# Optimization experiments

Hardware: AMD Instinct MI355X
Metric: run time of the kernel (lower is better)

The kernel has to match this reference:

```python
import jax, jax.numpy as jnp
import numpy as np

N = 100000
E = 1600000
H = 128
C = 40
BN_EPS = 1e-5


def setup_inputs() -> dict:
    key = jax.random.key(0)
    ks = jax.random.split(key, 8)
    x = jax.random.normal(ks[0], (N, H), dtype=jnp.float32)
    edge_index = jax.random.randint(ks[1], (2, E), 0, N, dtype=jnp.int64)
    # 3 GCN blocks (input + 2 hidden), all [H -> H] since in_channels == hidden_channels
    bn_gamma = jnp.ones((3, H), dtype=jnp.float32)
    bn_beta = jnp.zeros((3, H), dtype=jnp.float32)
    W = jax.random.normal(ks[2], (3, H, H), dtype=jnp.float32) / np.sqrt(H)
    b = jnp.zeros((3, H), dtype=jnp.float32)
    Wo = jax.random.normal(ks[3], (H, C), dtype=jnp.float32) / np.sqrt(H)
    bo = jnp.zeros((C,), dtype=jnp.float32)
    return {"x": x, "edge_index": edge_index, "bn_gamma": bn_gamma,
            "bn_beta": bn_beta, "W": W, "b": b, "Wo": Wo, "bo": bo}


def _gcn_norm(edge_index):
    # add self-loops, compute symmetric normalization deg^-1/2 * deg^-1/2
    loop = jnp.arange(N, dtype=edge_index.dtype)
    src = jnp.concatenate([edge_index[0], loop])  # [E+N]
    dst = jnp.concatenate([edge_index[1], loop])
    deg = jax.ops.segment_sum(jnp.ones_like(dst, dtype=jnp.float32), dst, num_segments=N)
    dinv = jnp.where(deg > 0, jax.lax.rsqrt(deg), 0.0)
    norm = dinv[src] * dinv[dst]  # [E+N]
    return src, dst, norm


def _block(x, src, dst, norm, gamma, beta, Wl, bl):
    # Dropout(p=0.6) in eval mode -> identity
    # BatchNorm (batch statistics, biased var, eps=1e-5)
    mean = jnp.mean(x, axis=0)
    var = jnp.mean(jnp.square(x - mean), axis=0)
    x = gamma * (x - mean) * jax.lax.rsqrt(var + BN_EPS) + beta
    # GCNConv: linear transform then normalized scatter-add aggregation
    h = x @ Wl  # [N, H]
    msg = h[src] * norm[:, None]  # [E+N, H] gather + scale
    out = jax.ops.segment_sum(msg, dst, num_segments=N) + bl
    return jax.nn.relu(out)


def reference(x, edge_index, bn_gamma, bn_beta, W, b, Wo, bo):
    src, dst, norm = _gcn_norm(edge_index)
    for i in range(3):
        x = _block(x, src, dst, norm, bn_gamma[i], bn_beta[i], W[i], b[i])
    logits = x @ Wo + bo  # [N, C]
    return jnp.squeeze(logits)
```

## Files before the change

kernel.cpp:

```cpp
#include <hip/hip_runtime.h>
#include <hip/hip_bf16.h>
#include <hip/hip_fp16.h>
#include <cstdint>

#define HDIM 128
#define BN_EPS 1e-5f
#define BUCKET_BITS 9
#define BSZ 512
#define CAP 10240
#define CHUNK 2048

typedef _Float16 hf2 __attribute__((ext_vector_type(2)));
typedef _Float16 hf8 __attribute__((ext_vector_type(8)));
typedef float f32x4 __attribute__((ext_vector_type(4)));

static inline size_t align256(size_t x) { return (x + 255) & ~size_t(255); }

__global__ void detect_zero(const int* __restrict__ ebuf, int* __restrict__ flag,
                            int* __restrict__ btot, int nbuck) {
    if (blockIdx.x == 1) {
        int i = threadIdx.x;
        if (i < nbuck) btot[i] = 0;
        return;
    }
    __shared__ int r[256];
    int tid = threadIdx.x;
    int o = 0;
    for (int i = tid; i < 4096; i += 256) o |= ebuf[2 * i + 1];
    r[tid] = o;
    __syncthreads();
    for (int s = 128; s > 0; s >>= 1) {
        if (tid < s) r[tid] |= r[tid + s];
        __syncthreads();
    }
    if (tid == 0) *flag = (r[0] == 0) ? 1 : 0;
}

__device__ __forceinline__ void bn_finalize_body(int blk, int t,
                                                 const float* __restrict__ part, int rows,
                                                 const float* __restrict__ gamma,
                                                 const float* __restrict__ beta,
                                                 const float* __restrict__ W,
                                                 _Float16* __restrict__ Wf,
                                                 float* __restrict__ hbp, int n) {
    int c = t & 127, h = t >> 7;
    float s = 0.f, s2 = 0.f;
    for (int b = h; b < rows; b += 2) {
        float2 v = ((const float2*)part)[(size_t)b * 128 + c];
        s += v.x; s2 += v.y;
    }
    __shared__ float rS[2][HDIM], rQ[2][HDIM];
    __shared__ float scs[HDIM], shs[HDIM];
    rS[h][c] = s; rQ[h][c] = s2;
    __syncthreads();
    if (h == 0) {
        s += rS[1][c]; s2 += rQ[1][c];
        float mean = s / n;
        float var = s2 / n - mean * mean;
        float sc = gamma[c] * rsqrtf(var + BN_EPS);
        scs[c] = sc;
        shs[c] = beta[c] - mean * sc;
    }
    __syncthreads();
    float acc = 0.f;
    int tbase = (c >> 4) * 4;
    int nlane = c & 15;
    int k0 = blk * 16 + h * 8;
#pragma unroll
    for (int kk = 0; kk < 8; ++kk) {
        int k = k0 + kk;
        float w = W[k * HDIM + c];
        int idx = (((tbase + (k >> 5)) * 64) + (((k >> 3) & 3) * 16 + nlane)) * 8 + (k & 7);
        Wf[idx] = (_Float16)(scs[k] * w);
        acc += shs[k] * w;
    }
    hbp[(blk * 2 + h) * HDIM + c] = acc;
}

__global__ __launch_bounds__(256) void hist_bn(const int* __restrict__ ebuf,
                                               const int* __restrict__ flag,
                                               int* __restrict__ btot,
                                               const float4* __restrict__ x4,
                                               float* __restrict__ part,
                                               int E, int n, int nbuck, int ghist, int nbn) {
    int t = threadIdx.x;
    if ((int)blockIdx.x < ghist) {
        __shared__ int bh[256];
        if (t < 256) bh[t] = 0;
        __syncthreads();
        int base = blockIdx.x * CHUNK;
        bool f = (*flag != 0);
#pragma unroll
        for (int i = 0; i < CHUNK / 256; ++i) {
            int e = base + i * 256 + t;
            if (e < E) {
                int d = f ? ebuf[2 * (E + e)] : ebuf[E + e];
                atomicAdd(&bh[d >> BUCKET_BITS], 1);
            }
        }
        __syncthreads();
        if (t < nbuck && bh[t] > 0) atomicAdd(&btot[t], bh[t]);
        return;
    }
    int b = blockIdx.x - ghist;
    int c4 = t & 31;
    int rsub = t >> 5;
    int rowsPer = (n + nbn - 1) / nbn;
    int r0 = b * rowsPer, r1 = min(r0 + rowsPer, n);
    float s[4] = {0.f, 0.f, 0.f, 0.f}, q[4] = {0.f, 0.f, 0.f, 0.f};
    for (int r = r0 + rsub; r < r1; r += 8) {
        float4 v = x4[(size_t)r * 32 + c4];
        s[0] += v.x; q[0] += v.x * v.x;
        s[1] += v.y; q[1] += v.y * v.y;
        s[2] += v.z; q[2] += v.z * v.z;
        s[3] += v.w; q[3] += v.w * v.w;
    }
    __shared__ float sS[8][HDIM], sQ[8][HDIM];
#pragma unroll
    for (int j = 0; j < 4; ++j) { sS[rsub][c4 * 4 + j] = s[j]; sQ[rsub][c4 * 4 + j] = q[j]; }
    __syncthreads();
    if (t < HDIM) {
        float ss = 0.f, qq = 0.f;
#pragma unroll
        for (int k = 0; k < 8; ++k) { ss += sS[k][t]; qq += sQ[k][t]; }
        ((float2*)part)[(size_t)b * 128 + t] = make_float2(ss, qq);
    }
}

__device__ __forceinline__ void reduce1_body(int blk, int t, const float* __restrict__ part,
                                             float* __restrict__ part2, int rows) {
    int per = (rows + 63) / 64;
    int b0 = blk * per, b1 = min(b0 + per, rows);
    float acc = 0.f;
    for (int r = b0; r < b1; ++r) acc += part[(size_t)r * 256 + t];
    part2[(size_t)blk * 256 + t] = acc;
}

__global__ __launch_bounds__(256) void bn_reduce1(const float* __restrict__ part,
                                                  float* __restrict__ part2, int rows) {
    reduce1_body(blockIdx.x, threadIdx.x, part, part2, rows);
}

__global__ __launch_bounds__(256) void scan_reduce(int* __restrict__ btot,
                                                   int* __restrict__ bbase,
                                                   int* __restrict__ bcursor,
                                                   const float* __restrict__ part,
                                                   float* __restrict__ part2,
                                                   int nbuck, int E, int bnrows) {
    int t = threadIdx.x;
    if (blockIdx.x > 0) {
        reduce1_body(blockIdx.x - 1, t, part, part2, bnrows);
        return;
    }
    int lane = t & 63, w = t >> 6;
    int v = (t < nbuck) ? btot[t] : 0;
    int x = v;
#pragma unroll
    for (int off = 1; off < 64; off <<= 1) {
        int y = __shfl_up(x, off);
        if (lane >= off) x += y;
    }
    __shared__ int ws4[4];
    if (lane == 63) ws4[w] = x;
    __syncthreads();
    int woff = 0;
#pragma unroll
    for (int k = 0; k < 4; ++k) if (k < w) woff += ws4[k];
    int ex = x + woff - v;
    if (t < nbuck) { bbase[t] = ex; bcursor[t] = ex; }
    if (t == 0) bbase[nbuck] = E;
}

__global__ __launch_bounds__(256) void scatter_fin(const int* __restrict__ ebuf,
                                                   const int* __restrict__ flag,
                                                   int* __restrict__ bcursor,
                                                   unsigned int* __restrict__ words,
                                                   int E, int nbuck, int gscat,
                                                   const float* __restrict__ part2,
                                                   const float* __restrict__ gamma,
                                                   const float* __restrict__ beta,
                                                   const float* __restrict__ W,
                                                   _Float16* __restrict__ Wf,
                                                   float* __restrict__ hbp, int n) {
    int t = threadIdx.x;
    if ((int)blockIdx.x >= gscat) {
        bn_finalize_body(blockIdx.x - gscat, t, part2, 64, gamma, beta, W, Wf, hbp, n);
        return;
    }
    __shared__ int bh[256];
    __shared__ int brange[256];
    if (t < 256) bh[t] = 0;
    __syncthreads();
    int base = blockIdx.x * CHUNK;
    bool f = (*flag != 0);
    int sv[CHUNK / 256], bk[CHUNK / 256], ld[CHUNK / 256];
#pragma unroll
    for (int i = 0; i < CHUNK / 256; ++i) {
        int e = base + i * 256 + t;
        bk[i] = -1;
        if (e < E) {
            int s = f ? ebuf[2 * e] : ebuf[e];
            int d = f ? ebuf[2 * (E + e)] : ebuf[E + e];
            sv[i] = s;
            bk[i] = d >> BUCKET_BITS;
            ld[i] = d & (BSZ - 1);
            atomicAdd(&bh[bk[i]], 1);
        }
    }
    __syncthreads();
    if (t < nbuck) {
        int c = bh[t];
        brange[t] = (c > 0) ? atomicAdd(&bcursor[t], c) : 0;
    }
    __syncthreads();
    if (t < 256) bh[t] = 0;
    __syncthreads();
#pragma unroll
    for (int i = 0; i < CHUNK / 256; ++i) {
        if (bk[i] >= 0) {
            int pos = brange[bk[i]] + atomicAdd(&bh[bk[i]], 1);
            words[pos] = (unsigned int)sv[i] | ((unsigned int)ld[i] << 17);
        }
    }
}

__global__ __launch_bounds__(256) void local_csr(const unsigned int* __restrict__ words,
                                                 const int* __restrict__ bbase,
                                                 int* __restrict__ csr_src,
                                                 int* __restrict__ row_ptr,
                                                 float* __restrict__ dinv, int n, int E) {
    __shared__ unsigned int warr[CAP];
    __shared__ int h[BSZ], ex[BSZ], cur[BSZ];
    __shared__ int ws4[4];
    int t = threadIdx.x;
    int b = blockIdx.x;
    int cb = bbase[b], ce = bbase[b + 1];
    int m = min(ce - cb, CAP);
    for (int i = t; i < m; i += 256) warr[i] = words[cb + i];
    if (t < 256) { h[t] = 0; h[t + 256] = 0; }
    __syncthreads();
    for (int i = t; i < m; i += 256) atomicAdd(&h[warr[i] >> 17], 1);
    __syncthreads();
    int a0 = h[2 * t], a1 = h[2 * t + 1];
    int sp = a0 + a1;
    int lane = t & 63, w = t >> 6;
    int x = sp;
#pragma unroll
    for (int off = 1; off < 64; off <<= 1) {
        int y = __shfl_up(x, off);
        if (lane >= off) x += y;
    }
    if (lane == 63) ws4[w] = x;
    __syncthreads();
    int woff = 0;
#pragma unroll
    for (int k = 0; k < 4; ++k) if (k < w) woff += ws4[k];
    int e0 = x + woff - sp;
    ex[2 * t] = e0; ex[2 * t + 1] = e0 + a0;
    cur[2 * t] = e0; cur[2 * t + 1] = e0 + a0;
    __syncthreads();
#pragma unroll
    for (int j = 0; j < 2; ++j) {
        int l = 2 * t + j;
        int gnode = (b << BUCKET_BITS) + l;
        if (gnode < n) {
            row_ptr[gnode] = cb + ex[l];
            dinv[gnode] = rsqrtf((float)(h[l] + 1));
        }
    }
    for (int i = t; i < m; i += 256) {
        unsigned int wv = warr[i];
        int l = wv >> 17;
        int pos = cb + atomicAdd(&cur[l], 1);
        csr_src[pos] = (int)(wv & 0x1FFFFu);
    }
    if (b == 0 && t == 0) row_ptr[n] = E;
}

__global__ __launch_bounds__(256) void bn_finalize_k(const float* __restrict__ part, int rows,
                                                     const float* __restrict__ gamma,
                                                     const float* __restrict__ beta,
                                                     const float* __restrict__ W,
                                                     _Float16* __restrict__ Wf,
                                                     float* __restrict__ hbp, int n) {
    bn_finalize_body(blockIdx.x, threadIdx.x, part, rows, gamma, beta, W, Wf, hbp, n);
}

#define GEMM_SMEM_BYTES (128 * 136 * 2 + 512 + 512)
template<bool F16SRC>
__device__ __forceinline__ void gemm_body(int bid, int t, unsigned char* sm,
                                          const void* __restrict__ xsrc,
                                          const _Float16* __restrict__ Wf,
                                          const float* __restrict__ hbp,
                                          const float* __restrict__ dinv,
                                          __half* __restrict__ Q, int n) {
    constexpr int XS = 136;
    _Float16* xs = (_Float16*)sm;
    float* dvs = (float*)(sm + 128 * 136 * 2);
    float* hbs = (float*)(sm + 128 * 136 * 2 + 512);
    int rowBase = bid * 128;
    if (t < 128) {
        int gr = rowBase + t;
        dvs[t] = (gr < n) ? dinv[gr] : 0.f;
        float hsum = 0.f;
#pragma unroll
        for (int b = 0; b < 16; ++b) hsum += hbp[b * HDIM + t];
        hbs[t] = hsum;
    }
    int wid = t >> 6, l = t & 63;
    int wm = wid >> 1, wn = wid & 1;
    const hf8* wf8 = (const hf8*)Wf;
    hf8 bf[4][4];
#pragma unroll
    for (int i = 0; i < 4; ++i)
#pragma unroll
        for (int kk = 0; kk < 4; ++kk)
            bf[i][kk] = wf8[((4 * wn + i) * 4 + kk) * 64 + l];
    if (F16SRC) {
        const uint4* xg = (const uint4*)xsrc;
#pragma unroll
        for (int i = 0; i < 8; ++i) {
            int idx = t + 256 * i;
            int row = idx >> 4, o4 = idx & 15;
            int gr = rowBase + row;
            uint4 v = make_uint4(0, 0, 0, 0);
            if (gr < n) v = xg[(size_t)gr * 16 + o4];
            *(uint4*)&xs[row * XS + o4 * 8] = v;
        }
    } else {
        const float4* xg = (const float4*)xsrc;
#pragma unroll
        for (int i = 0; i < 16; ++i) {
            int idx = t + 256 * i;
            int row = idx >> 5, o = idx & 31;
            int gr = rowBase + row;
            float4 v = make_float4(0.f, 0.f, 0.f, 0.f);
            if (gr < n) v = xg[(size_t)gr * 32 + o];
            hf2 a; a.x = (_Float16)v.x; a.y = (_Float16)v.y;
            hf2 b; b.x = (_Float16)v.z; b.y = (_Float16)v.w;
            *(hf2*)&xs[row * XS + o * 4]     = a;
            *(hf2*)&xs[row * XS + o * 4 + 2] = b;
        }
    }
    __syncthreads();
    f32x4 acc[4][4] = {};
    int mlane = l & 15, agrp = l >> 4;
#pragma unroll
    for (int kk = 0; kk < 4; ++kk) {
        hf8 af[4];
#pragma unroll
        for (int mt = 0; mt < 4; ++mt)
            af[mt] = *(const hf8*)&xs[(64 * wm + 16 * mt + mlane) * XS + 32 * kk + 8 * agrp];
#pragma unroll
        for (int mt = 0; mt < 4; ++mt)
#pragma unroll
            for (int i = 0; i < 4; ++i)
                acc[mt][i] = __builtin_amdgcn_mfma_f32_16x16x32_f16(af[mt], bf[i][kk],
                                                                    acc[mt][i], 0, 0, 0);
    }
#pragma unroll
    for (int mt = 0; mt < 4; ++mt) {
        int r0 = 64 * wm + 16 * mt + agrp * 4;
#pragma unroll
        for (int j = 0; j < 4; ++j) {
            int r = r0 + j;
            int grow = rowBase + r;
            if (grow < n) {
                float dv = dvs[r];
#pragma unroll
                for (int i = 0; i < 4; ++i) {
                    int c = 16 * (4 * wn + i) + mlane;
                    Q[(size_t)grow * 128 + c] = __float2half(dv * (acc[mt][i][j] + hbs[c]));
                }
            }
        }
    }
}

template<bool F16SRC>
__global__ __launch_bounds__(256) void gemm_mfma(const void* __restrict__ xsrc,
                                                 const _Float16* __restrict__ Wf,
                                                 const float* __restrict__ hbp,
                                                 const float* __restrict__ dinv,
                                                 __half* __restrict__ Q, int n) {
    __shared__ __align__(16) unsigned char sm[GEMM_SMEM_BYTES];
    gemm_body<F16SRC>(blockIdx.x, threadIdx.x, sm, xsrc, Wf, hbp, dinv, Q, n);
}

__device__ __forceinline__ void add8(float acc[8], uint4 v) {
    const __half2* p = (const __half2*)&v;
#pragma unroll
    for (int j = 0; j < 4; ++j) {
        float2 f = __half22float2(p[j]);
        acc[2 * j]     += f.x;
        acc[2 * j + 1] += f.y;
    }
}

__global__ __launch_bounds__(256) void agg_kernel(const __half* __restrict__ h,
                                                  const int* __restrict__ row_ptr,
                                                  const int* __restrict__ csr_src,
                                                  const float* __restrict__ dinv,
                                                  const float* __restrict__ bias,
                                                  __half* __restrict__ xn,
                                                  float* __restrict__ part, int n) {
    int t = threadIdx.x;
    int lane16 = t & 15;
    int g = t >> 4;
    int d = blockIdx.x * 16 + g;
    bool active = (d < n);
    const uint4* h4 = (const uint4*)h;
    float v[8];
#pragma unroll
    for (int j = 0; j < 8; ++j) v[j] = 0.f;
    if (active) {
        float acc[8];
        {
            uint4 hv = h4[(size_t)d * 16 + lane16];
            const __half2* p = (const __half2*)&hv;
#pragma unroll
            for (int j = 0; j < 4; ++j) {
                float2 f = __half22float2(p[j]);
                acc[2 * j]     = f.x;
                acc[2 * j + 1] = f.y;
            }
        }
        int e0 = row_ptr[d], e1 = row_ptr[d + 1];
        int e = e0;
        for (; e + 16 <= e1; e += 16) {
            int idx[16];
#pragma unroll
            for (int i = 0; i < 16; ++i) idx[i] = csr_src[e + i];
            uint4 vv[16];
#pragma unroll
            for (int i = 0; i < 16; ++i) vv[i] = h4[(size_t)idx[i] * 16 + lane16];
#pragma unroll
            for (int i = 0; i < 16; ++i) add8(acc, vv[i]);
        }
        int rem = e1 - e;
        if (rem > 0) {
            int idx[16];
#pragma unroll
            for (int i = 0; i < 16; ++i)
                if (i < rem) idx[i] = csr_src[e + i];
            uint4 vv[16];
#pragma unroll
            for (int i = 0; i < 16; ++i)
                if (i < rem) vv[i] = h4[(size_t)idx[i] * 16 + lane16];
#pragma unroll
            for (int i = 0; i < 16; ++i)
                if (i < rem) add8(acc, vv[i]);
        }
        float dv = dinv[d];
        const float4* bb = (const float4*)(bias + lane16 * 8);
        float4 b0 = bb[0], b1 = bb[1];
        v[0] = fmaxf(fmaf(dv, acc[0], b0.x), 0.f);
        v[1] = fmaxf(fmaf(dv, acc[1], b0.y), 0.f);
        v[2] = fmaxf(fmaf(dv, acc[2], b0.z), 0.f);
        v[3] = fmaxf(fmaf(dv, acc[3], b0.w), 0.f);
        v[4] = fmaxf(fmaf(dv, acc[4], b1.x), 0.f);
        v[5] = fmaxf(fmaf(dv, acc[5], b1.y), 0.f);
        v[6] = fmaxf(fmaf(dv, acc[6], b1.z), 0.f);
        v[7] = fmaxf(fmaf(dv, acc[7], b1.w), 0.f);
        union { uint4 u; __half2 h2[4]; } o;
        o.h2[0] = __floats2half2_rn(v[0], v[1]);
        o.h2[1] = __floats2half2_rn(v[2], v[3]);
        o.h2[2] = __floats2half2_rn(v[4], v[5]);
        o.h2[3] = __floats2half2_rn(v[6], v[7]);
        ((uint4*)xn)[(size_t)d * 16 + lane16] = o.u;
    }
    if (part) {
        __shared__ float redS[16][HDIM];
        __shared__ float redQ[16][HDIM];
#pragma unroll
        for (int j = 0; j < 8; ++j) {
            redS[g][lane16 * 8 + j] = v[j];
            redQ[g][lane16 * 8 + j] = v[j] * v[j];
        }
        __syncthreads();
        if (t < HDIM) {
            float s = 0.f, q = 0.f;
#pragma unroll
            for (int k = 0; k < 16; ++k) { s += redS[k][t]; q += redQ[k][t]; }
            ((float2*)part)[(size_t)blockIdx.x * 128 + t] = make_float2(s, q);
        }
    }
}

__global__ __launch_bounds__(320) void gemm_out(const __half* __restrict__ x,
                                                const float* __restrict__ Wo,
                                                const float* __restrict__ bo,
                                                float* __restrict__ out, int n, int C) {
    __shared__ __align__(16) float wls[HDIM * 40];
    __shared__ __align__(16) float xs[32 * HDIM];
    __shared__ float bos[40];
    int t = threadIdx.x;
    for (int i = t; i < HDIM * 40; i += 320) wls[i] = Wo[i];
    if (t < 40) bos[t] = bo[t];
    int c = t % 40, lr = t / 40;
    int rowBase = blockIdx.x * 32;
    const uint4* xg = (const uint4*)x;
    for (int i = t; i < 512; i += 320) {
        int row = i >> 4, o4 = i & 15;
        int gr = rowBase + row;
        uint4 v = make_uint4(0, 0, 0, 0);
        if (gr < n) v = xg[(size_t)gr * 16 + o4];
        union { uint4 u; __half2 h2[4]; } cv; cv.u = v;
        float2 f0 = __half22float2(cv.h2[0]);
        float2 f1 = __half22float2(cv.h2[1]);
        float2 f2 = __half22float2(cv.h2[2]);
        float2 f3 = __half22float2(cv.h2[3]);
        ((float4*)xs)[i * 2]     = make_float4(f0.x, f0.y, f1.x, f1.y);
        ((float4*)xs)[i * 2 + 1] = make_float4(f2.x, f2.y, f3.x, f3.y);
    }
    __syncthreads();
    const float4* xsr0 = (const float4*)(xs + (lr + 0) * HDIM);
    const float4* xsr1 = (const float4*)(xs + (lr + 8) * HDIM);
    const float4* xsr2 = (const float4*)(xs + (lr + 16) * HDIM);
    const float4* xsr3 = (const float4*)(xs + (lr + 24) * HDIM);
    float acc0 = 0.f, acc1 = 0.f, acc2 = 0.f, acc3 = 0.f;
#pragma unroll 4
    for (int k4 = 0; k4 < 32; ++k4) {
        float4 xv0 = xsr0[k4], xv1 = xsr1[k4], xv2 = xsr2[k4], xv3 = xsr3[k4];
#define OSTEP(kk, e0, e1, e2, e3)                          \
        {                                                   \
            float wv = wls[(k4 * 4 + kk) * 40 + c];         \
            acc0 = fmaf(e0, wv, acc0);                      \
            acc1 = fmaf(e1, wv, acc1);                      \
            acc2 = fmaf(e2, wv, acc2);                      \
            acc3 = fmaf(e3, wv, acc3);                      \
        }
        OSTEP(0, xv0.x, xv1.x, xv2.x, xv3.x)
        OSTEP(1, xv0.y, xv1.y, xv2.y, xv3.y)
        OSTEP(2, xv0.z, xv1.z, xv2.z, xv3.z)
        OSTEP(3, xv0.w, xv1.w, xv2.w, xv3.w)
#undef OSTEP
    }
    float bb = bos[c];
    int g0 = rowBase + lr;
    if (g0 < n)      out[(size_t)g0 * 40 + c]        = acc0 + bb;
    if (g0 + 8 < n)  out[(size_t)(g0 + 8) * 40 + c]  = acc1 + bb;
    if (g0 + 16 < n) out[(size_t)(g0 + 16) * 40 + c] = acc2 + bb;
    if (g0 + 24 < n) out[(size_t)(g0 + 24) * 40 + c] = acc3 + bb;
}

extern "C" void kernel_launch(void* const* d_in, const int* in_sizes, int n_in,
                              void* d_out, int out_size, void* d_ws, size_t ws_size,
                              hipStream_t stream) {
    const float* x_in  = (const float*)d_in[0];
    const int*   ebuf  = (const int*)d_in[1];
    const float* gamma = (const float*)d_in[2];
    const float* beta  = (const float*)d_in[3];
    const float* Wall  = (const float*)d_in[4];
    const float* ball  = (const float*)d_in[5];
    const float* Wo    = (const float*)d_in[6];
    const float* bo    = (const float*)d_in[7];
    float* out = (float*)d_out;
    const int N = in_sizes[0] / HDIM;
    const int E = in_sizes[1] / 2;
    const int C = 40;

    char* base = (char*)d_ws;
    size_t off = 0;
    auto alloc = [&](size_t bytes) -> void* {
        void* p = base + off;
        off = align256(off + bytes);
        return p;
    };
    const int g_agg = (N + 15) / 16;
    const int g_bn0 = 1024;
    const int nbuck = (N + BSZ - 1) >> BUCKET_BITS;
    int part_rows = (g_agg > g_bn0) ? g_agg : g_bn0;
    __half*       Xh0     = (__half*)alloc((size_t)N * HDIM * 2);
    __half*       Xh1     = (__half*)alloc((size_t)N * HDIM * 2);
    __half*       Q       = (__half*)alloc((size_t)N * HDIM * 2);
    int*          csr_src = (int*)alloc((size_t)E * 4);
    unsigned int* words   = (unsigned int*)alloc((size_t)E * 4);
    float*        dinv    = (float*)alloc((size_t)N * 4);
    int*          row_ptr = (int*)alloc((size_t)(N + 1) * 4);
    float*        part    = (float*)alloc((size_t)part_rows * 256 * 4);
    float*        part2   = (float*)alloc((size_t)64 * 256 * 4);
    _Float16*     Wf      = (_Float16*)alloc((size_t)HDIM * HDIM * 2);
    float*        hbp     = (float*)alloc((size_t)16 * HDIM * 4);
    int*          btot    = (int*)alloc((size_t)256 * 4);
    int*          bbase   = (int*)alloc((size_t)256 * 4);
    int*          bcursor = (int*)alloc((size_t)256 * 4);
    int*          flag    = (int*)alloc(4);

    int ghist = (E + CHUNK - 1) / CHUNK;
    int gg = (N + 127) / 128;

    detect_zero<<<2, 256, 0, stream>>>(ebuf, flag, btot, nbuck);
    hist_bn<<<ghist + g_bn0, 256, 0, stream>>>(ebuf, flag, btot, (const float4*)x_in,
                                               part, E, N, nbuck, ghist, g_bn0);
    scan_reduce<<<65, 256, 0, stream>>>(btot, bbase, bcursor, part, part2, nbuck, E, g_bn0);
    scatter_fin<<<ghist + 8, 256, 0, stream>>>(ebuf, flag, bcursor, words, E, nbuck, ghist,
                                               part2, gamma, beta, Wall, Wf, hbp, N);
    local_csr<<<nbuck, 256, 0, stream>>>(words, bbase, csr_src, row_ptr, dinv, N, E);
    gemm_mfma<false><<<gg, 256, 0, stream>>>(x_in, Wf, hbp, dinv, Q, N);

    for (int l = 0; l < 3; ++l) {
        __half* xn = (l == 0) ? Xh0 : (l == 1) ? Xh1 : Xh0;
        if (l > 0) {
            const void* xc = (l == 1) ? (const void*)Xh0 : (const void*)Xh1;
            bn_reduce1<<<64, 256, 0, stream>>>(part, part2, g_agg);
            bn_finalize_k<<<8, 256, 0, stream>>>(part2, 64, gamma + l * HDIM, beta + l * HDIM,
                                                 Wall + (size_t)l * HDIM * HDIM, Wf, hbp, N);
            gemm_mfma<true><<<gg, 256, 0, stream>>>(xc, Wf, hbp, dinv, Q, N);
        }
        float* statp = (l < 2) ? part : nullptr;
        agg_kernel<<<g_agg, 256, 0, stream>>>(Q, row_ptr, csr_src, dinv,
                                              ball + l * HDIM, xn, statp, N);
    }
    gemm_out<<<(N + 31) / 32, 320, 0, stream>>>(Xh0, Wo, bo, out, N, C);
}
```

Baseline: 424.7 us.

## Shard feature matrices into column slices for cache-local edge aggregation

Feature and message matrices are stored as 8 column shards of 16 halves each, laid out shard-major. Aggregation now runs one thread per node per shard, with edge indices staged in LDS, so each gather only touches a roughly 3 MB shard that can stay resident in cache. BatchNorm statistics move out of the aggregation kernel into a separate shard-aware reduction, which adds an extra pass over the activations. The GEMM and output kernels are updated to read and write the sharded layout.

```diff
diff --git a/kernel.cpp b/kernel.cpp
--- a/kernel.cpp
+++ b/kernel.cpp
@@ -9,6 +9,8 @@
 #define BSZ 512
 #define CAP 10240
 #define CHUNK 2048
+#define NSHARD 8
+#define AGG_LDSE 6144
 
 typedef _Float16 hf2 __attribute__((ext_vector_type(2)));
 typedef _Float16 hf8 __attribute__((ext_vector_type(8)));
@@ -136,11 +138,6 @@
     part2[(size_t)blk * 256 + t] = acc;
 }
 
-__global__ __launch_bounds__(256) void bn_reduce1(const float* __restrict__ part,
-                                                  float* __restrict__ part2, int rows) {
-    reduce1_body(blockIdx.x, threadIdx.x, part, part2, rows);
-}
-
 __global__ __launch_bounds__(256) void scan_reduce(int* __restrict__ btot,
                                                    int* __restrict__ bbase,
                                                    int* __restrict__ bcursor,
@@ -286,19 +283,80 @@
     bn_finalize_body(blockIdx.x, threadIdx.x, part, rows, gamma, beta, W, Wf, hbp, n);
 }
 
-#define GEMM_SMEM_BYTES (128 * 136 * 2 + 512 + 512)
-template<bool F16SRC>
-__device__ __forceinline__ void gemm_body(int bid, int t, unsigned char* sm,
-                                          const void* __restrict__ xsrc,
-                                          const _Float16* __restrict__ Wf,
-                                          const float* __restrict__ hbp,
-                                          const float* __restrict__ dinv,
-                                          __half* __restrict__ Q, int n) {
+__global__ __launch_bounds__(256) void bn_stats_shard(const __half* __restrict__ x,
+                                                      float* __restrict__ parth, int n) {
+    int t = threadIdx.x;
+    int s = blockIdx.x & 7, b = blockIdx.x >> 3;
+    int chunk = (n + 127) / 128;
+    int r0 = b * chunk, r1 = min(r0 + chunk, n);
+    int hh = t & 1;
+    const uint4* xg = (const uint4*)x;
+    size_t sb = (size_t)s * n;
+    float sa[8] = {}, qa[8] = {};
+    for (int node = r0 + (t >> 1); node < r1; node += 128) {
+        uint4 v = xg[(sb + node) * 2 + hh];
+        const __half2* p = (const __half2*)&v;
+#pragma unroll
+        for (int j = 0; j < 4; ++j) {
+            float2 f = __half22float2(p[j]);
+            sa[2 * j] += f.x;     qa[2 * j] += f.x * f.x;
+            sa[2 * j + 1] += f.y; qa[2 * j + 1] += f.y * f.y;
+        }
+    }
+#pragma unroll
+    for (int off = 32; off >= 2; off >>= 1) {
+#pragma unroll
+        for (int j = 0; j < 8; ++j) {
+            sa[j] += __shfl_down(sa[j], off);
+            qa[j] += __shfl_down(qa[j], off);
+        }
+    }
+    __shared__ float redS[4][2][8], redQ[4][2][8];
+    int wv = t >> 6, lane = t & 63;
+    if (lane < 2) {
+#pragma unroll
+        for (int j = 0; j < 8; ++j) { redS[wv][lane][j] = sa[j]; redQ[wv][lane][j] = qa[j]; }
+    }
+    __syncthreads();
+    if (t < 16) {
+        int h2 = t >> 3, j = t & 7;
+        float ss = 0.f, qq = 0.f;
+#pragma unroll
+        for (int w = 0; w < 4; ++w) { ss += redS[w][h2][j]; qq += redQ[w][h2][j]; }
+        float* row = parth + (size_t)(s * 128 + b) * 32;
+        row[t * 2] = ss; row[t * 2 + 1] = qq;
+    }
+}
+
+__global__ __launch_bounds__(256) void reduce_shard(const float* __restrict__ parth,
+                                                    float* __restrict__ part2) {
+    int t = threadIdx.x, s = blockIdx.x;
+    int k = t & 31, r0 = t >> 5;
+    float acc = 0.f;
+    for (int r = r0; r < 128; r += 8) acc += parth[(size_t)(s * 128 + r) * 32 + k];
+    __shared__ float red[8][32];
+    red[r0][k] = acc;
+    __syncthreads();
+    if (t < 32) {
+        float v = 0.f;
+#pragma unroll
+        for (int i = 0; i < 8; ++i) v += red[i][t];
+        part2[s * 32 + t] = v;
+    }
+}
+
+template<bool F16SHARD>
+__global__ __launch_bounds__(256) void gemm_mfma(const void* __restrict__ xsrc,
+                                                 const _Float16* __restrict__ Wf,
+                                                 const float* __restrict__ hbp,
+                                                 const float* __restrict__ dinv,
+                                                 __half* __restrict__ Q, int n) {
     constexpr int XS = 136;
-    _Float16* xs = (_Float16*)sm;
-    float* dvs = (float*)(sm + 128 * 136 * 2);
-    float* hbs = (float*)(sm + 128 * 136 * 2 + 512);
-    int rowBase = bid * 128;
+    __shared__ _Float16 xs[128 * XS];
+    __shared__ float dvs[128];
+    __shared__ float hbs[128];
+    int t = threadIdx.x;
+    int rowBase = blockIdx.x * 128;
     if (t < 128) {
         int gr = rowBase + t;
         dvs[t] = (gr < n) ? dinv[gr] : 0.f;
@@ -316,15 +374,16 @@
 #pragma unroll
         for (int kk = 0; kk < 4; ++kk)
             bf[i][kk] = wf8[((4 * wn + i) * 4 + kk) * 64 + l];
-    if (F16SRC) {
+    if (F16SHARD) {
         const uint4* xg = (const uint4*)xsrc;
 #pragma unroll
         for (int i = 0; i < 8; ++i) {
             int idx = t + 256 * i;
             int row = idx >> 4, o4 = idx & 15;
             int gr = rowBase + row;
+            int s = o4 >> 1, hh = o4 & 1;
             uint4 v = make_uint4(0, 0, 0, 0);
-            if (gr < n) v = xg[(size_t)gr * 16 + o4];
+            if (gr < n) v = xg[((size_t)s * n + gr) * 2 + hh];
             *(uint4*)&xs[row * XS + o4 * 8] = v;
         }
     } else {
@@ -370,121 +429,84 @@
 #pragma unroll
                 for (int i = 0; i < 4; ++i) {
                     int c = 16 * (4 * wn + i) + mlane;
-                    Q[(size_t)grow * 128 + c] = __float2half(dv * (acc[mt][i][j] + hbs[c]));
+                    Q[((size_t)(4 * wn + i) * n + grow) * 16 + mlane] =
+                        __float2half(dv * (acc[mt][i][j] + hbs[c]));
                 }
             }
         }
     }
 }
 
-template<bool F16SRC>
-__global__ __launch_bounds__(256) void gemm_mfma(const void* __restrict__ xsrc,
-                                                 const _Float16* __restrict__ Wf,
-                                                 const float* __restrict__ hbp,
-                                                 const float* __restrict__ dinv,
-                                                 __half* __restrict__ Q, int n) {
-    __shared__ __align__(16) unsigned char sm[GEMM_SMEM_BYTES];
-    gemm_body<F16SRC>(blockIdx.x, threadIdx.x, sm, xsrc, Wf, hbp, dinv, Q, n);
-}
-
-__device__ __forceinline__ void add8(float acc[8], uint4 v) {
-    const __half2* p = (const __half2*)&v;
+__device__ __forceinline__ void add32h(float acc[16], uint4 a, uint4 b) {
+    const __half2* p = (const __half2*)&a;
+    const __half2* q = (const __half2*)&b;
 #pragma unroll
     for (int j = 0; j < 4; ++j) {
         float2 f = __half22float2(p[j]);
-        acc[2 * j]     += f.x;
-        acc[2 * j + 1] += f.y;
-    }
-}
-
-__global__ __launch_bounds__(256) void agg_kernel(const __half* __restrict__ h,
-                                                  const int* __restrict__ row_ptr,
-                                                  const int* __restrict__ csr_src,
-                                                  const float* __restrict__ dinv,
-                                                  const float* __restrict__ bias,
-                                                  __half* __restrict__ xn,
-                                                  float* __restrict__ part, int n) {
-    int t = threadIdx.x;
-    int lane16 = t & 15;
-    int g = t >> 4;
-    int d = blockIdx.x * 16 + g;
-    bool active = (d < n);
-    const uint4* h4 = (const uint4*)h;
-    float v[8];
-#pragma unroll
-    for (int j = 0; j < 8; ++j) v[j] = 0.f;
-    if (active) {
-        float acc[8];
-        {
-            uint4 hv = h4[(size_t)d * 16 + lane16];
-            const __half2* p = (const __half2*)&hv;
-#pragma unroll
-            for (int j = 0; j < 4; ++j) {
-                float2 f = __half22float2(p[j]);
-                acc[2 * j]     = f.x;
-                acc[2 * j + 1] = f.y;
-            }
-        }
-        int e0 = row_ptr[d], e1 = row_ptr[d + 1];
-        int e = e0;
-        for (; e + 16 <= e1; e += 16) {
-            int idx[16];
-#pragma unroll
-            for (int i = 0; i < 16; ++i) idx[i] = csr_src[e + i];
-            uint4 vv[16];
-#pragma unroll
-            for (int i = 0; i < 16; ++i) vv[i] = h4[(size_t)idx[i] * 16 + lane16];
-#pragma unroll
-            for (int i = 0; i < 16; ++i) add8(acc, vv[i]);
-        }
-        int rem = e1 - e;
-        if (rem > 0) {
-            int idx[16];
-#pragma unroll
-            for (int i = 0; i < 16; ++i)
-                if (i < rem) idx[i] = csr_src[e + i];
-            uint4 vv[16];
-#pragma unroll
-            for (int i = 0; i < 16; ++i)
-                if (i < rem) vv[i] = h4[(size_t)idx[i] * 16 + lane16];
-#pragma unroll
-            for (int i = 0; i < 16; ++i)
-                if (i < rem) add8(acc, vv[i]);
-        }
-        float dv = dinv[d];
-        const float4* bb = (const float4*)(bias + lane16 * 8);
-        float4 b0 = bb[0], b1 = bb[1];
-        v[0] = fmaxf(fmaf(dv, acc[0], b0.x), 0.f);
-        v[1] = fmaxf(fmaf(dv, acc[1], b0.y), 0.f);
-        v[2] = fmaxf(fmaf(dv, acc[2], b0.z), 0.f);
-        v[3] = fmaxf(fmaf(dv, acc[3], b0.w), 0.f);
-        v[4] = fmaxf(fmaf(dv, acc[4], b1.x), 0.f);
-        v[5] = fmaxf(fmaf(dv, acc[5], b1.y), 0.f);
-        v[6] = fmaxf(fmaf(dv, acc[6], b1.z), 0.f);
-        v[7] = fmaxf(fmaf(dv, acc[7], b1.w), 0.f);
-        union { uint4 u; __half2 h2[4]; } o;
-        o.h2[0] = __floats2half2_rn(v[0], v[1]);
-        o.h2[1] = __floats2half2_rn(v[2], v[3]);
-        o.h2[2] = __floats2half2_rn(v[4], v[5]);
-        o.h2[3] = __floats2half2_rn(v[6], v[7]);
-        ((uint4*)xn)[(size_t)d * 16 + lane16] = o.u;
-    }
-    if (part) {
-        __shared__ float redS[16][HDIM];
-        __shared__ float redQ[16][HDIM];
-#pragma unroll
-        for (int j = 0; j < 8; ++j) {
-            redS[g][lane16 * 8 + j] = v[j];
-            redQ[g][lane16 * 8 + j] = v[j] * v[j];
-        }
-        __syncthreads();
-        if (t < HDIM) {
-            float s = 0.f, q = 0.f;
-#pragma unroll
-            for (int k = 0; k < 16; ++k) { s += redS[k][t]; q += redQ[k][t]; }
-            ((float2*)part)[(size_t)blockIdx.x * 128 + t] = make_float2(s, q);
-        }
-    }
+        acc[2 * j] += f.x; acc[2 * j + 1] += f.y;
+    }
+#pragma unroll
+    for (int j = 0; j < 4; ++j) {
+        float2 f = __half22float2(q[j]);
+        acc[8 + 2 * j] += f.x; acc[8 + 2 * j + 1] += f.y;
+    }
+}
+
+__global__ __launch_bounds__(256) void agg_shard(const __half* __restrict__ Qm,
+                                                 const int* __restrict__ row_ptr,
+                                                 const int* __restrict__ csr_src,
+                                                 const float* __restrict__ dinv,
+                                                 const float* __restrict__ bias,
+                                                 __half* __restrict__ xn, int n) {
+    __shared__ int sidx[AGG_LDSE];
+    int t = threadIdx.x;
+    int s = blockIdx.x & 7;
+    int n0 = (blockIdx.x >> 3) * 256;
+    int nEnd = min(n0 + 256, n);
+    int R0 = row_ptr[n0], R1 = row_ptr[nEnd];
+    int m = min(R1 - R0, AGG_LDSE);
+    for (int i = t; i < m; i += 256) sidx[i] = csr_src[R0 + i];
+    __syncthreads();
+    int node = n0 + t;
+    if (node >= n) return;
+    const uint4* q4 = (const uint4*)Qm;
+    size_t sb = (size_t)s * n;
+    float acc[16];
+#pragma unroll
+    for (int j = 0; j < 16; ++j) acc[j] = 0.f;
+    {
+        uint4 a = q4[(sb + node) * 2], b = q4[(sb + node) * 2 + 1];
+        add32h(acc, a, b);
+    }
+    int e = row_ptr[node] - R0, e1 = row_ptr[node + 1] - R0;
+    for (; e + 4 <= e1; e += 4) {
+        int i0 = (e < AGG_LDSE) ? sidx[e] : csr_src[R0 + e];
+        int i1 = (e + 1 < AGG_LDSE) ? sidx[e + 1] : csr_src[R0 + e + 1];
+        int i2 = (e + 2 < AGG_LDSE) ? sidx[e + 2] : csr_src[R0 + e + 2];
+        int i3 = (e + 3 < AGG_LDSE) ? sidx[e + 3] : csr_src[R0 + e + 3];
+        uint4 a0 = q4[(sb + i0) * 2], b0 = q4[(sb + i0) * 2 + 1];
+        uint4 a1 = q4[(sb + i1) * 2], b1 = q4[(sb + i1) * 2 + 1];
+        uint4 a2 = q4[(sb + i2) * 2], b2 = q4[(sb + i2) * 2 + 1];
+        uint4 a3 = q4[(sb + i3) * 2], b3 = q4[(sb + i3) * 2 + 1];
+        add32h(acc, a0, b0); add32h(acc, a1, b1);
+        add32h(acc, a2, b2); add32h(acc, a3, b3);
+    }
+    for (; e < e1; ++e) {
+        int i0 = (e < AGG_LDSE) ? sidx[e] : csr_src[R0 + e];
+        uint4 a = q4[(sb + i0) * 2], b = q4[(sb + i0) * 2 + 1];
+        add32h(acc, a, b);
+    }
+    float dv = dinv[node];
+    const float4* bp = (const float4*)(bias + s * 16);
+    float4 b4[4] = {bp[0], bp[1], bp[2], bp[3]};
+    const float* bf = (const float*)b4;
+    union { uint4 u[2]; __half2 h2[8]; } o;
+#pragma unroll
+    for (int j = 0; j < 8; ++j)
+        o.h2[j] = __floats2half2_rn(fmaxf(fmaf(dv, acc[2 * j], bf[2 * j]), 0.f),
+                                    fmaxf(fmaf(dv, acc[2 * j + 1], bf[2 * j + 1]), 0.f));
+    ((uint4*)xn)[(sb + node) * 2]     = o.u[0];
+    ((uint4*)xn)[(sb + node) * 2 + 1] = o.u[1];
 }
 
 __global__ __launch_bounds__(320) void gemm_out(const __half* __restrict__ x,
@@ -503,8 +525,9 @@
     for (int i = t; i < 512; i += 320) {
         int row = i >> 4, o4 = i & 15;
         int gr = rowBase + row;
+        int s = o4 >> 1, hh = o4 & 1;
         uint4 v = make_uint4(0, 0, 0, 0);
-        if (gr < n) v = xg[(size_t)gr * 16 + o4];
+        if (gr < n) v = xg[((size_t)s * n + gr) * 2 + hh];
         union { uint4 u; __half2 h2[4]; } cv; cv.u = v;
         float2 f0 = __half22float2(cv.h2[0]);
         float2 f1 = __half22float2(cv.h2[1]);
@@ -567,10 +590,8 @@
         off = align256(off + bytes);
         return p;
     };
-    const int g_agg = (N + 15) / 16;
     const int g_bn0 = 1024;
     const int nbuck = (N + BSZ - 1) >> BUCKET_BITS;
-    int part_rows = (g_agg > g_bn0) ? g_agg : g_bn0;
     __half*       Xh0     = (__half*)alloc((size_t)N * HDIM * 2);
     __half*       Xh1     = (__half*)alloc((size_t)N * HDIM * 2);
     __half*       Q       = (__half*)alloc((size_t)N * HDIM * 2);
@@ -578,7 +599,8 @@
     unsigned int* words   = (unsigned int*)alloc((size_t)E * 4);
     float*        dinv    = (float*)alloc((size_t)N * 4);
     int*          row_ptr = (int*)alloc((size_t)(N + 1) * 4);
-    float*        part    = (float*)alloc((size_t)part_rows * 256 * 4);
+    float*        part    = (float*)alloc((size_t)g_bn0 * 256 * 4);
+    float*        parth   = (float*)alloc((size_t)1024 * 32 * 4);
     float*        part2   = (float*)alloc((size_t)64 * 256 * 4);
     _Float16*     Wf      = (_Float16*)alloc((size_t)HDIM * HDIM * 2);
     float*        hbp     = (float*)alloc((size_t)16 * HDIM * 4);
@@ -589,6 +611,7 @@
 
     int ghist = (E + CHUNK - 1) / CHUNK;
     int gg = (N + 127) / 128;
+    int gagg = ((N + 255) / 256) * NSHARD;
 
     detect_zero<<<2, 256, 0, stream>>>(ebuf, flag, btot, nbuck);
     hist_bn<<<ghist + g_bn0, 256, 0, stream>>>(ebuf, flag, btot, (const float4*)x_in,
@@ -602,15 +625,15 @@
     for (int l = 0; l < 3; ++l) {
         __half* xn = (l == 0) ? Xh0 : (l == 1) ? Xh1 : Xh0;
         if (l > 0) {
-            const void* xc = (l == 1) ? (const void*)Xh0 : (const void*)Xh1;
-            bn_reduce1<<<64, 256, 0, stream>>>(part, part2, g_agg);
-            bn_finalize_k<<<8, 256, 0, stream>>>(part2, 64, gamma + l * HDIM, beta + l * HDIM,
+            const __half* xc = (l == 1) ? Xh0 : Xh1;
+            bn_stats_shard<<<1024, 256, 0, stream>>>(xc, parth, N);
+            reduce_shard<<<8, 256, 0, stream>>>(parth, part2);
+            bn_finalize_k<<<8, 256, 0, stream>>>(part2, 1, gamma + l * HDIM, beta + l * HDIM,
                                                  Wall + (size_t)l * HDIM * HDIM, Wf, hbp, N);
             gemm_mfma<true><<<gg, 256, 0, stream>>>(xc, Wf, hbp, dinv, Q, N);
         }
-        float* statp = (l < 2) ? part : nullptr;
-        agg_kernel<<<g_agg, 256, 0, stream>>>(Q, row_ptr, csr_src, dinv,
-                                              ball + l * HDIM, xn, statp, N);
+        agg_shard<<<gagg, 256, 0, stream>>>(Q, row_ptr, csr_src, dinv,
+                                            ball + l * HDIM, xn, N);
     }
     gemm_out<<<(N + 31) / 32, 320, 0, stream>>>(Xh0, Wo, bo, out, N, C);
 }
```

Measured after the change: 465.7 us. +9.7%, slower.
